# Kernel optimization log

Measured on AMD Instinct MI355X. Metric: run time of the kernel, lower is better.

Reference implementation:

```python
import jax, jax.numpy as jnp
import numpy as np

D_MODEL = 1024
NHEAD = 16
D_HEAD = D_MODEL // NHEAD
D_FF = 2 * D_MODEL
EPS = 1e-5


def setup_inputs() -> dict:
    key = jax.random.key(0)
    ks = jax.random.split(key, 12)
    s = 1.0 / np.sqrt(D_MODEL)
    x = jax.random.normal(ks[0], (4, 1024, D_MODEL), dtype=jnp.float32)
    # per-head projections stacked: [H, d_model, d_head] (x @ W layout)
    wq = jax.random.normal(ks[1], (NHEAD, D_MODEL, D_HEAD), dtype=jnp.float32) * s
    bq = jnp.zeros((NHEAD, D_HEAD), dtype=jnp.float32)
    wk = jax.random.normal(ks[2], (NHEAD, D_MODEL, D_HEAD), dtype=jnp.float32) * s
    bk = jnp.zeros((NHEAD, D_HEAD), dtype=jnp.float32)
    wv = jax.random.normal(ks[3], (NHEAD, D_MODEL, D_HEAD), dtype=jnp.float32) * s
    bv = jnp.zeros((NHEAD, D_HEAD), dtype=jnp.float32)
    wo_w = jax.random.normal(ks[4], (D_MODEL, D_MODEL), dtype=jnp.float32) * s
    wo_b = jnp.zeros((D_MODEL,), dtype=jnp.float32)
    ff1_w = jax.random.normal(ks[5], (D_MODEL, D_FF), dtype=jnp.float32) * s
    ff1_b = jnp.zeros((D_FF,), dtype=jnp.float32)
    ff2_w = jax.random.normal(ks[6], (D_FF, D_MODEL), dtype=jnp.float32) * (1.0 / np.sqrt(D_FF))
    ff2_b = jnp.zeros((D_MODEL,), dtype=jnp.float32)
    g1 = jnp.ones((D_MODEL,), dtype=jnp.float32)
    b1 = jnp.zeros((D_MODEL,), dtype=jnp.float32)
    g2 = jnp.ones((D_MODEL,), dtype=jnp.float32)
    b2 = jnp.zeros((D_MODEL,), dtype=jnp.float32)
    return dict(x=x, wq=wq, bq=bq, wk=wk, bk=bk, wv=wv, bv=bv,
                wo_w=wo_w, wo_b=wo_b, g1=g1, b1=b1,
                ff1_w=ff1_w, ff1_b=ff1_b, ff2_w=ff2_w, ff2_b=ff2_b,
                g2=g2, b2=b2)


def manual_layernorm(x, gamma, beta):
    # faithful to source: (x - mean) / (std + eps), std unbiased=False
    mean = jnp.mean(x, axis=-1, keepdims=True)
    std = jnp.sqrt(jnp.mean((x - mean) ** 2, axis=-1, keepdims=True))
    return gamma * (x - mean) / (std + EPS) + beta


def reference(x, wq, bq, wk, bk, wv, bv, wo_w, wo_b, g1, b1,
              ff1_w, ff1_b, ff2_w, ff2_b, g2, b2):
    B, S, D = x.shape
    # per-head projections, vectorized over heads: [B,H,S,d_head]
    q = jnp.einsum('bsd,hdk->bhsk', x, wq) + bq[None, :, None, :]
    k = jnp.einsum('bsd,hdk->bhsk', x, wk) + bk[None, :, None, :]
    v = jnp.einsum('bsd,hdk->bhsk', x, wv) + bv[None, :, None, :]
    scores = jnp.einsum('bhsk,bhtk->bhst', q, k) / jnp.sqrt(jnp.float32(D_HEAD))
    weights = jax.nn.softmax(scores, axis=-1)
    attn = jnp.einsum('bhst,bhtk->bhsk', weights, v)
    # concat heads back to [B,S,D]
    concat = jnp.transpose(attn, (0, 2, 1, 3)).reshape(B, S, D)
    proj = concat @ wo_w + wo_b
    h = manual_layernorm(x + proj, g1, b1)
    ff = jax.nn.relu(h @ ff1_w + ff1_b) @ ff2_w + ff2_b
    return manual_layernorm(h + ff, g2, b2)
```

## Files before the change

kernel.cpp:

```cpp
#include <hip/hip_runtime.h>
#include <hip/hip_bf16.h>

typedef __attribute__((ext_vector_type(8))) short bf16x8;
typedef __attribute__((ext_vector_type(4))) float f32x4;
using bf16 = __hip_bfloat16;

#define NTOK 4096
#define EPS_LN 1e-5f
#define QSCL 0.1803368801111244f

enum { EPI_F32 = 0, EPI_QKV = 1, EPI_RELU_BF16 = 2, EPI_BF16 = 3 };

#define VM8 asm volatile("s_waitcnt vmcnt(8)" ::: "memory")
#define VM0 asm volatile("s_waitcnt vmcnt(0)" ::: "memory")
#define LGKM0 asm volatile("s_waitcnt lgkmcnt(0)" ::: "memory")
#define SCHED0 __builtin_amdgcn_sched_barrier(0)
#define NOVM
#define DSRO(dst, ad, off) \
  asm volatile("ds_read_b128 %0, %1 offset:" #off : "=v"(dst) : "v"(ad))

__device__ inline void gload_lds16(const void* g, void* l) {
  __builtin_amdgcn_global_load_lds(
      (const __attribute__((address_space(1))) char*)g,
      (__attribute__((address_space(3))) char*)l, 16, 0, 0);
}

__device__ inline unsigned ldsoff(const void* p) {
  return (unsigned)(size_t)(const __attribute__((address_space(3))) char*)p;
}

__device__ inline unsigned short f2bfu(float x) {
  bf16 h = __float2bfloat16(x);
  return __builtin_bit_cast(unsigned short, h);
}
__device__ inline bf16 to_bf16(float v) { return __float2bfloat16(v); }
__device__ inline bf16 to_bf16(bf16 v) { return v; }

__device__ inline unsigned cvtpk(float lo, float hi) {
  unsigned r;
  asm volatile("v_cvt_pk_bf16_f32 %0, %1, %2" : "=v"(r) : "v"(lo), "v"(hi));
  return r;
}
__device__ inline float bu2f(unsigned short u) {
  unsigned v = (unsigned)u << 16;
  return __builtin_bit_cast(float, v);
}


__global__ __launch_bounds__(256) void cvt_bf16_kernel(const float* __restrict__ src,
                                                       bf16* __restrict__ dst, int n4) {
  int i = blockIdx.x * 256 + threadIdx.x;
  if (i >= n4) return;
  float4 v = ((const float4*)src)[i];
  ushort4 o;
  o.x = f2bfu(v.x); o.y = f2bfu(v.y); o.z = f2bfu(v.z); o.w = f2bfu(v.w);
  ((ushort4*)dst)[i] = o;
}

template <typename ST>
__global__ __launch_bounds__(256) void transpose_cvt(const ST* __restrict__ src,
                                                     bf16* __restrict__ dst, int R, int C) {
  __shared__ bf16 tile[32][33];
  int o = blockIdx.z;
  int r0 = blockIdx.y * 32, c0 = blockIdx.x * 32;
  int tx = threadIdx.x & 31, ty = threadIdx.x >> 5;
  const ST* s = src + (size_t)o * R * C;
  bf16* d = dst + (size_t)o * R * C;
#pragma unroll
  for (int i = 0; i < 32; i += 8)
    tile[ty + i][tx] = to_bf16(s[(size_t)(r0 + ty + i) * C + (c0 + tx)]);
  __syncthreads();
#pragma unroll
  for (int i = 0; i < 32; i += 8)
    d[(size_t)(c0 + ty + i) * R + (r0 + tx)] = tile[tx][ty + i];
}

__global__ __launch_bounds__(256) void pack_bias_kernel(const float* __restrict__ bq,
                                                        const float* __restrict__ bk,
                                                        const float* __restrict__ bv,
                                                        float* __restrict__ out) {
  int i = blockIdx.x * 256 + threadIdx.x;
  if (i >= 3072) return;
  out[i] = (i < 1024) ? bq[i] : (i < 2048 ? bk[i - 1024] : bv[i - 2048]);
}


#define STG(KOFF, DD) { _Pragma("unroll") for (int q = 0; q < 4; ++q) { \
    gload_lds16(gA0 + (KOFF) + (size_t)(q * 32) * lda2, \
                sAb + (DD) * 16384 + q * 4096 + w * 1024); \
    gload_lds16(gB0 + (KOFF) + (size_t)(q * 32) * ldb2, \
                sBb + (DD) * 16384 + q * 4096 + w * 1024); } }

#define TILE(OFFLIT, STG_, VMS) { \
  _Pragma("unroll") for (int i = 0; i < 4; ++i) { \
    DSRO(a[i][0], adA[i][0], OFFLIT); \
    DSRO(a[i][1], adA[i][1], OFFLIT); \
  } \
  _Pragma("unroll") for (int j = 0; j < 4; ++j) { \
    DSRO(b[j][0], adB[j][0], OFFLIT); \
    DSRO(b[j][1], adB[j][1], OFFLIT); \
  } \
  LGKM0; SCHED0; \
  __builtin_amdgcn_s_barrier(); \
  STG_; \
  __builtin_amdgcn_s_setprio(1); \
  _Pragma("unroll") for (int i = 0; i < 4; ++i) \
  _Pragma("unroll") for (int j = 0; j < 4; ++j) \
  _Pragma("unroll") for (int kk = 0; kk < 2; ++kk) \
    acc[i][j] = __builtin_amdgcn_mfma_f32_16x16x32_bf16( \
        a[i][kk], b[j][kk], acc[i][j], 0, 0, 0); \
  __builtin_amdgcn_s_setprio(0); \
  VMS; \
  __builtin_amdgcn_s_barrier(); }

__global__ __launch_bounds__(256, 2) void gemm128(
    const bf16* __restrict__ A, int lda,
    const bf16* __restrict__ Bt, int ldb,
    int M, int N, int K,
    int nbm, int nbn,
    const float* __restrict__ bias,
    float* __restrict__ Cf, bf16* __restrict__ Cb,
    bf16* __restrict__ Qd, bf16* __restrict__ Kd, bf16* __restrict__ Vd,
    int mode) {
  __shared__ bf16 sA[2][128][64];
  __shared__ bf16 sB[2][128][64];
  const int nwg = nbm * nbn;
  const int orig = blockIdx.x;
  const int wgid = (orig % 8) * (nwg / 8) + orig / 8;
  const int bm = wgid / nbn, bn = wgid % nbn;
  const int tid = threadIdx.x;
  const int w = tid >> 6, lane = tid & 63;
  const int wm = w >> 1, wn = w & 1;
  const int ri = lane & 15, kg = lane >> 4;
  const bf16* Ab = A + (size_t)bm * 128 * lda;
  const bf16* Bb = Bt + (size_t)bn * 128 * ldb;
  const int NT = K / 64;
  const size_t lda2 = (size_t)lda * 2, ldb2 = (size_t)ldb * 2;
  char* sAb = (char*)&sA[0][0][0];
  char* sBb = (char*)&sB[0][0][0];

  unsigned adA[4][2], adB[4][2];
  const unsigned sA0 = ldsoff(sAb), sB0 = ldsoff(sBb);
#pragma unroll
  for (int i = 0; i < 4; ++i) {
    int row = wm * 64 + i * 16 + ri;
    unsigned swz = (unsigned)((row & 7) << 4);
    adA[i][0] = sA0 + row * 128 + ((kg * 16) ^ swz);
    adA[i][1] = sA0 + row * 128 + ((64 + kg * 16) ^ swz);
  }
#pragma unroll
  for (int j = 0; j < 4; ++j) {
    int row = wn * 64 + j * 16 + ri;
    unsigned swz = (unsigned)((row & 7) << 4);
    adB[j][0] = sB0 + row * 128 + ((kg * 16) ^ swz);
    adB[j][1] = sB0 + row * 128 + ((64 + kg * 16) ^ swz);
  }

  const int r0 = tid >> 3;
  const int cb0 = ((tid & 7) * 16) ^ ((r0 & 7) << 4);
  const char* gA0 = (const char*)Ab + (size_t)r0 * lda2 + cb0;
  const char* gB0 = (const char*)Bb + (size_t)r0 * ldb2 + cb0;

  f32x4 acc[4][4] = {};
  bf16x8 a[4][2], b[4][2];

  STG(0, 0) STG(128, 1)
  VM8;
  __builtin_amdgcn_s_barrier();

  const int niter = NT / 2 - 1;
  for (int it = 0; it < niter; ++it) {
    TILE(0,     STG(256, 0), VM8)
    TILE(16384, STG(384, 1), VM8)
    gA0 += 256; gB0 += 256;
  }
  TILE(0,     , VM0)
  TILE(16384, , NOVM)

  const int colbase = bn * 128 + wn * 64 + ri;
  float bv4[4];
#pragma unroll
  for (int nf = 0; nf < 4; ++nf)
    bv4[nf] = bias ? bias[colbase + nf * 16] : 0.f;

  if (mode == EPI_QKV) {
    int col0 = bn * 128 + wn * 64;
    int which = col0 >> 10, hh = (col0 >> 6) & 15;
    bf16* dst = (which == 0) ? Qd : (which == 1) ? Kd : Vd;
    float scl = (which == 0) ? QSCL : 1.0f;
#pragma unroll
    for (int mf = 0; mf < 4; ++mf)
#pragma unroll
      for (int r = 0; r < 4; ++r) {
        int row = bm * 128 + wm * 64 + mf * 16 + kg * 4 + r;
        int b2 = row >> 10, s = row & 1023;
        bf16* o = dst + (((size_t)(b2 * 16 + hh)) * 1024 + s) * 64;
#pragma unroll
        for (int nf = 0; nf < 4; ++nf)
          o[nf * 16 + ri] = __float2bfloat16((acc[mf][nf][r] + bv4[nf]) * scl);
      }
  } else if (mode == EPI_F32) {
#pragma unroll
    for (int mf = 0; mf < 4; ++mf)
#pragma unroll
      for (int r = 0; r < 4; ++r) {
        int row = bm * 128 + wm * 64 + mf * 16 + kg * 4 + r;
        float* o = Cf + (size_t)row * N + colbase;
#pragma unroll
        for (int nf = 0; nf < 4; ++nf) o[nf * 16] = acc[mf][nf][r] + bv4[nf];
      }
  } else if (mode == EPI_RELU_BF16) {
#pragma unroll
    for (int mf = 0; mf < 4; ++mf)
#pragma unroll
      for (int r = 0; r < 4; ++r) {
        int row = bm * 128 + wm * 64 + mf * 16 + kg * 4 + r;
        bf16* o = Cb + (size_t)row * N + colbase;
#pragma unroll
        for (int nf = 0; nf < 4; ++nf) {
          float v = acc[mf][nf][r] + bv4[nf];
          o[nf * 16] = __float2bfloat16(v > 0.f ? v : 0.f);
        }
      }
  } else {
#pragma unroll
    for (int mf = 0; mf < 4; ++mf)
#pragma unroll
      for (int r = 0; r < 4; ++r) {
        int row = bm * 128 + wm * 64 + mf * 16 + kg * 4 + r;
        bf16* o = Cb + (size_t)row * N + colbase;
#pragma unroll
        for (int nf = 0; nf < 4; ++nf)
          o[nf * 16] = __float2bfloat16(acc[mf][nf][r] + bv4[nf]);
      }
  }
}

__global__ __launch_bounds__(256, 4) void attn_kernel(
    const bf16* __restrict__ Qb, const bf16* __restrict__ Kb,
    const bf16* __restrict__ Vs, bf16* __restrict__ Ob) {
  __shared__ bf16 KV[2][2][64][64];
  __shared__ bf16 Ps[4][16][64];
  const int orig = blockIdx.x;
  const int blk = (orig & 7) * 128 + (orig >> 3);
  const int bh = blk >> 4, qt = blk & 15;
  const int bb = bh >> 4, hh = bh & 15;
  const int tid = threadIdx.x, w = tid >> 6, lane = tid & 63;
  const int ri = lane & 15, kg = lane >> 4, r8 = lane >> 3;
  const int cb = ((lane & 7) * 16) ^ ((r8 & 7) << 4);
  const unsigned rsw = (unsigned)((ri & 7) << 4);
  const bf16* qp = Qb + (size_t)bh * 65536;
  const bf16* kp = Kb + (size_t)bh * 65536;
  const bf16* vp = Vs + (size_t)bh * 65536;
  const int q0 = qt * 64 + w * 16;
  const int c0 = w * 2, c1 = c0 + 1;

  unsigned offk0 = (unsigned)((kg * 16) ^ (int)rsw);
  unsigned offk1 = (unsigned)((64 + kg * 16) ^ (int)rsw);
  unsigned adF[4][2];
  const unsigned kv0 = ldsoff(&KV[0][0][0][0]);
#pragma unroll
  for (int n = 0; n < 4; ++n) {
    unsigned row = (unsigned)((n * 16 + ri) * 128);
    adF[n][0] = kv0 + row + offk0;
    adF[n][1] = kv0 + row + offk1;
  }
  const unsigned ps0 = ldsoff(&Ps[0][0][0]) + (unsigned)(w * 2048 + ri * 128);
  unsigned adPr[2] = {ps0 + offk0, ps0 + offk1};
  char* pwb = (char*)&Ps[0][0][0] + w * 2048 + ri * 128;
  char* adPw[4];
#pragma unroll
  for (int n = 0; n < 4; ++n)
    adPw[n] = pwb + ((n * 32 + kg * 8) ^ (int)rsw);

  bf16x8 qf[2];
  qf[0] = *(const bf16x8*)(qp + (size_t)(q0 + ri) * 64 + kg * 8);
  qf[1] = *(const bf16x8*)(qp + (size_t)(q0 + ri) * 64 + 32 + kg * 8);

  bf16x8 ones;
#pragma unroll
  for (int e = 0; e < 8; ++e) ones[e] = (short)0x3F80;

  f32x4 oacc[4] = {};
  f32x4 lacc = {};
  float mrun = -1e30f;

#define ASTAGE(T, D) { \
    gload_lds16((const char*)(kp + (size_t)((T) * 64 + c0 * 8 + r8) * 64) + cb, \
                (char*)KV + (D) * 16384 + c0 * 1024); \
    gload_lds16((const char*)(kp + (size_t)((T) * 64 + c1 * 8 + r8) * 64) + cb, \
                (char*)KV + (D) * 16384 + c1 * 1024); \
    gload_lds16((const char*)(vp + (size_t)(c0 * 8 + r8) * 1024 + (T) * 64) + cb, \
                (char*)KV + (D) * 16384 + 8192 + c0 * 1024); \
    gload_lds16((const char*)(vp + (size_t)(c1 * 8 + r8) * 1024 + (T) * 64) + cb, \
                (char*)KV + (D) * 16384 + 8192 + c1 * 1024); }

#define ATILE(KOFF, VOFF, STG_, ENDSYNC) { \
  bf16x8 kf0[4], kf1[4]; \
  _Pragma("unroll") for (int n = 0; n < 4; ++n) { \
    DSRO(kf0[n], adF[n][0], KOFF); \
    DSRO(kf1[n], adF[n][1], KOFF); \
  } \
  STG_; \
  LGKM0; SCHED0; \
  f32x4 sac[4] = {}; \
  _Pragma("unroll") for (int n = 0; n < 4; ++n) { \
    sac[n] = __builtin_amdgcn_mfma_f32_16x16x32_bf16(kf0[n], qf[0], sac[n], 0, 0, 0); \
    sac[n] = __builtin_amdgcn_mfma_f32_16x16x32_bf16(kf1[n], qf[1], sac[n], 0, 0, 0); \
  } \
  float mx[4]; \
  _Pragma("unroll") for (int n = 0; n < 4; ++n) \
    mx[n] = fmaxf(fmaxf(sac[n][0], sac[n][1]), fmaxf(sac[n][2], sac[n][3])); \
  float mt16 = fmaxf(fmaxf(mx[0], mx[1]), fmaxf(mx[2], mx[3])); \
  if (!__all(mt16 - mrun <= 8.f)) { \
    float mrow = fmaxf(mt16, __shfl_xor(mt16, 16)); \
    mrow = fmaxf(mrow, __shfl_xor(mrow, 32)); \
    float mnew = fmaxf(mrun, mrow); \
    float corr = exp2f(mrun - mnew); \
    mrun = mnew; \
    float cr[4]; \
    _Pragma("unroll") for (int r = 0; r < 4; ++r) cr[r] = __shfl(corr, kg * 4 + r); \
    _Pragma("unroll") for (int n = 0; n < 4; ++n) { \
      oacc[n][0] *= cr[0]; oacc[n][1] *= cr[1]; \
      oacc[n][2] *= cr[2]; oacc[n][3] *= cr[3]; \
    } \
    lacc[0] *= cr[0]; lacc[1] *= cr[1]; lacc[2] *= cr[2]; lacc[3] *= cr[3]; \
  } \
  _Pragma("unroll") for (int n = 0; n < 4; ++n) { \
    uint2 pk; \
    pk.x = cvtpk(exp2f(sac[n][0] - mrun), exp2f(sac[n][1] - mrun)); \
    pk.y = cvtpk(exp2f(sac[n][2] - mrun), exp2f(sac[n][3] - mrun)); \
    *(uint2*)adPw[n] = pk; \
  } \
  LGKM0; \
  bf16x8 pf0, pf1, vf0[4], vf1[4]; \
  DSRO(pf0, adPr[0], 0); \
  DSRO(pf1, adPr[1], 0); \
  _Pragma("unroll") for (int n = 0; n < 4; ++n) { \
    DSRO(vf0[n], adF[n][0], VOFF); \
    DSRO(vf1[n], adF[n][1], VOFF); \
  } \
  LGKM0; SCHED0; \
  _Pragma("unroll") for (int n = 0; n < 4; ++n) { \
    oacc[n] = __builtin_amdgcn_mfma_f32_16x16x32_bf16(pf0, vf0[n], oacc[n], 0, 0, 0); \
    oacc[n] = __builtin_amdgcn_mfma_f32_16x16x32_bf16(pf1, vf1[n], oacc[n], 0, 0, 0); \
  } \
  lacc = __builtin_amdgcn_mfma_f32_16x16x32_bf16(pf0, ones, lacc, 0, 0, 0); \
  lacc = __builtin_amdgcn_mfma_f32_16x16x32_bf16(pf1, ones, lacc, 0, 0, 0); \
  ENDSYNC }

#define SYNCT { VM0; __syncthreads(); }

  ASTAGE(0, 0);
  VM0;
  __syncthreads();

  for (int tt = 0; tt < 7; ++tt) {
    const int t2 = tt * 2;
    ATILE(0,     8192,  ASTAGE(t2 + 1, 1), SYNCT)
    ATILE(16384, 24576, ASTAGE(t2 + 2, 0), SYNCT)
  }
  ATILE(0,     8192,  ASTAGE(15, 1), SYNCT)
  ATILE(16384, 24576, ,              )

  float ivr[4];
#pragma unroll
  for (int r = 0; r < 4; ++r) ivr[r] = 1.f / lacc[r];
#pragma unroll
  for (int r = 0; r < 4; ++r) {
    int s = q0 + kg * 4 + r;
    size_t base = ((size_t)(bb * 1024 + s)) * 1024 + hh * 64;
#pragma unroll
    for (int n = 0; n < 4; ++n)
      Ob[base + n * 16 + ri] = __float2bfloat16(oacc[n][r] * ivr[r]);
  }
#undef ASTAGE
#undef ATILE
#undef SYNCT
}

__global__ __launch_bounds__(256) void ln_bb(
    const bf16* __restrict__ a, const bf16* __restrict__ b,
    const float* __restrict__ gamma, const float* __restrict__ beta,
    float* __restrict__ out_f32, bf16* __restrict__ out_bf16) {
  int row = blockIdx.x;
  int tid = threadIdx.x;
  ushort4 au = ((const ushort4*)(a + (size_t)row * 1024))[tid];
  ushort4 bu = ((const ushort4*)(b + (size_t)row * 1024))[tid];
  float4 z;
  z.x = bu2f(au.x) + bu2f(bu.x);
  z.y = bu2f(au.y) + bu2f(bu.y);
  z.z = bu2f(au.z) + bu2f(bu.z);
  z.w = bu2f(au.w) + bu2f(bu.w);
  float s = z.x + z.y + z.z + z.w;
  float ss = z.x * z.x + z.y * z.y + z.z * z.z + z.w * z.w;
#pragma unroll
  for (int o = 32; o >= 1; o >>= 1) { s += __shfl_xor(s, o); ss += __shfl_xor(ss, o); }
  __shared__ float red[8];
  int wid = tid >> 6;
  if ((tid & 63) == 0) { red[wid] = s; red[4 + wid] = ss; }
  __syncthreads();
  s = red[0] + red[1] + red[2] + red[3];
  ss = red[4] + red[5] + red[6] + red[7];
  float mean = s * (1.f / 1024.f);
  float var = ss * (1.f / 1024.f) - mean * mean;
  var = var > 0.f ? var : 0.f;
  float inv = 1.f / (sqrtf(var) + EPS_LN);
  float4 g = ((const float4*)gamma)[tid];
  float4 be = ((const float4*)beta)[tid];
  float4 y;
  y.x = (z.x - mean) * inv * g.x + be.x;
  y.y = (z.y - mean) * inv * g.y + be.y;
  y.z = (z.z - mean) * inv * g.z + be.z;
  y.w = (z.w - mean) * inv * g.w + be.w;
  ((float4*)(out_f32 + (size_t)row * 1024))[tid] = y;
  ushort4 o;
  o.x = f2bfu(y.x); o.y = f2bfu(y.y); o.z = f2bfu(y.z); o.w = f2bfu(y.w);
  ((ushort4*)(out_bf16 + (size_t)row * 1024))[tid] = o;
}

__global__ __launch_bounds__(256) void ln_fb(
    const float* __restrict__ a, const bf16* __restrict__ b,
    const float* __restrict__ gamma, const float* __restrict__ beta,
    float* __restrict__ out_f32) {
  int row = blockIdx.x;
  int tid = threadIdx.x;
  float4 av = ((const float4*)(a + (size_t)row * 1024))[tid];
  ushort4 bu = ((const ushort4*)(b + (size_t)row * 1024))[tid];
  float4 z;
  z.x = av.x + bu2f(bu.x);
  z.y = av.y + bu2f(bu.y);
  z.z = av.z + bu2f(bu.z);
  z.w = av.w + bu2f(bu.w);
  float s = z.x + z.y + z.z + z.w;
  float ss = z.x * z.x + z.y * z.y + z.z * z.z + z.w * z.w;
#pragma unroll
  for (int o = 32; o >= 1; o >>= 1) { s += __shfl_xor(s, o); ss += __shfl_xor(ss, o); }
  __shared__ float red[8];
  int wid = tid >> 6;
  if ((tid & 63) == 0) { red[wid] = s; red[4 + wid] = ss; }
  __syncthreads();
  s = red[0] + red[1] + red[2] + red[3];
  ss = red[4] + red[5] + red[6] + red[7];
  float mean = s * (1.f / 1024.f);
  float var = ss * (1.f / 1024.f) - mean * mean;
  var = var > 0.f ? var : 0.f;
  float inv = 1.f / (sqrtf(var) + EPS_LN);
  float4 g = ((const float4*)gamma)[tid];
  float4 be = ((const float4*)beta)[tid];
  float4 y;
  y.x = (z.x - mean) * inv * g.x + be.x;
  y.y = (z.y - mean) * inv * g.y + be.y;
  y.z = (z.z - mean) * inv * g.z + be.z;
  y.w = (z.w - mean) * inv * g.w + be.w;
  ((float4*)(out_f32 + (size_t)row * 1024))[tid] = y;
}

extern "C" void kernel_launch(void* const* d_in, const int* in_sizes, int n_in,
                              void* d_out, int out_size, void* d_ws, size_t ws_size,
                              hipStream_t stream) {
  const float* x = (const float*)d_in[0];
  const float* wq = (const float*)d_in[1];
  const float* bq = (const float*)d_in[2];
  const float* wk = (const float*)d_in[3];
  const float* bk = (const float*)d_in[4];
  const float* wv = (const float*)d_in[5];
  const float* bv = (const float*)d_in[6];
  const float* wo_w = (const float*)d_in[7];
  const float* wo_b = (const float*)d_in[8];
  const float* g1 = (const float*)d_in[9];
  const float* b1 = (const float*)d_in[10];
  const float* ff1w = (const float*)d_in[11];
  const float* ff1b = (const float*)d_in[12];
  const float* ff2w = (const float*)d_in[13];
  const float* ff2b = (const float*)d_in[14];
  const float* g2 = (const float*)d_in[15];
  const float* b2 = (const float*)d_in[16];

  char* ws = (char*)d_ws;
  size_t off = 0;
  auto alloc = [&](size_t bytes) {
    char* p = ws + off;
    off += (bytes + 255) & ~(size_t)255;
    return p;
  };
  bf16* xb = (bf16*)alloc((size_t)NTOK * 1024 * 2);
  bf16* wqkvt = (bf16*)alloc((size_t)3072 * 1024 * 2);
  bf16* wot = (bf16*)alloc((size_t)1024 * 1024 * 2);
  bf16* ff1t = (bf16*)alloc((size_t)2048 * 1024 * 2);
  bf16* ff2t = (bf16*)alloc((size_t)1024 * 2048 * 2);
  float* qkvbias = (float*)alloc(3072 * 4);
  bf16* qbuf = (bf16*)alloc((size_t)64 * 1024 * 64 * 2);
  bf16* kbuf = (bf16*)alloc((size_t)64 * 1024 * 64 * 2);
  bf16* vbuf = (bf16*)alloc((size_t)64 * 1024 * 64 * 2);
  bf16* vtb = (bf16*)alloc((size_t)64 * 64 * 1024 * 2);
  bf16* attnb = (bf16*)alloc((size_t)NTOK * 1024 * 2);
  bf16* projb = (bf16*)alloc((size_t)NTOK * 1024 * 2);
  bf16* hb = (bf16*)alloc((size_t)NTOK * 1024 * 2);
  bf16* ff1o = qbuf;
  float* hbuf = (float*)d_out;

  cvt_bf16_kernel<<<(NTOK * 1024 / 4 + 255) / 256, 256, 0, stream>>>(x, xb, NTOK * 1024 / 4);
  transpose_cvt<float><<<dim3(2, 32, 16), 256, 0, stream>>>(wq, wqkvt, 1024, 64);
  transpose_cvt<float><<<dim3(2, 32, 16), 256, 0, stream>>>(wk, wqkvt + 1024 * 1024, 1024, 64);
  transpose_cvt<float><<<dim3(2, 32, 16), 256, 0, stream>>>(wv, wqkvt + 2 * 1024 * 1024, 1024, 64);
  transpose_cvt<float><<<dim3(32, 32, 1), 256, 0, stream>>>(wo_w, wot, 1024, 1024);
  transpose_cvt<float><<<dim3(64, 32, 1), 256, 0, stream>>>(ff1w, ff1t, 1024, 2048);
  transpose_cvt<float><<<dim3(32, 64, 1), 256, 0, stream>>>(ff2w, ff2t, 2048, 1024);
  pack_bias_kernel<<<12, 256, 0, stream>>>(bq, bk, bv, qkvbias);

  gemm128<<<768, 256, 0, stream>>>(xb, 1024, wqkvt, 1024, 4096, 3072, 1024,
                                   32, 24, qkvbias,
                                   nullptr, nullptr, qbuf, kbuf, vbuf, EPI_QKV);
  transpose_cvt<bf16><<<dim3(2, 32, 64), 256, 0, stream>>>(vbuf, vtb, 1024, 64);
  attn_kernel<<<dim3(1024), 256, 0, stream>>>(qbuf, kbuf, vtb, attnb);
  gemm128<<<256, 256, 0, stream>>>(attnb, 1024, wot, 1024, 4096, 1024, 1024,
                                   32, 8, wo_b,
                                   nullptr, projb, nullptr, nullptr, nullptr, EPI_BF16);
  ln_bb<<<4096, 256, 0, stream>>>(xb, projb, g1, b1, hbuf, hb);
  gemm128<<<512, 256, 0, stream>>>(hb, 1024, ff1t, 1024, 4096, 2048, 1024,
                                   32, 16, ff1b,
                                   nullptr, ff1o, nullptr, nullptr, nullptr, EPI_RELU_BF16);
  gemm128<<<256, 256, 0, stream>>>(ff1o, 2048, ff2t, 2048, 4096, 1024, 2048,
                                   32, 8, ff2b,
                                   nullptr, projb, nullptr, nullptr, nullptr, EPI_BF16);
  ln_fb<<<4096, 256, 0, stream>>>(hbuf, projb, g2, b2, (float*)d_out);
}
```

Baseline: 167.3 us.

## Replace pipelined GEMM with single-buffer loop, add 128x64 GEMM, unify LayerNorm

The double-buffered, hand-scheduled GEMM main loop is replaced by a simple single-buffer loop that syncs every k-tile, with occupancy raised to 3 blocks. A new 128x64-tile GEMM is added for the N=1024 output projection and FF2 so they launch 512 blocks instead of 256. The second LayerNorm now reuses ln_bb and takes the bf16 h as its residual instead of the fp32 copy, and the fp32 h buffer is no longer written. Loads and MFMA no longer overlap, which risks exposing memory latency, and the residual path loses fp32 precision.

```diff
diff --git a/kernel.cpp b/kernel.cpp
--- a/kernel.cpp
+++ b/kernel.cpp
@@ -9,13 +9,11 @@
 #define EPS_LN 1e-5f
 #define QSCL 0.1803368801111244f
 
-enum { EPI_F32 = 0, EPI_QKV = 1, EPI_RELU_BF16 = 2, EPI_BF16 = 3 };
-
-#define VM8 asm volatile("s_waitcnt vmcnt(8)" ::: "memory")
-#define VM0 asm volatile("s_waitcnt vmcnt(0)" ::: "memory")
+enum { EPI_QKV = 1, EPI_RELU_BF16 = 2 };
+
 #define LGKM0 asm volatile("s_waitcnt lgkmcnt(0)" ::: "memory")
 #define SCHED0 __builtin_amdgcn_sched_barrier(0)
-#define NOVM
+#define VM0 asm volatile("s_waitcnt vmcnt(0)" ::: "memory")
 #define DSRO(dst, ad, off) \
   asm volatile("ds_read_b128 %0, %1 offset:" #off : "=v"(dst) : "v"(ad))
 
@@ -85,45 +83,20 @@
 }
 
 
-#define STG(KOFF, DD) { _Pragma("unroll") for (int q = 0; q < 4; ++q) { \
-    gload_lds16(gA0 + (KOFF) + (size_t)(q * 32) * lda2, \
-                sAb + (DD) * 16384 + q * 4096 + w * 1024); \
-    gload_lds16(gB0 + (KOFF) + (size_t)(q * 32) * ldb2, \
-                sBb + (DD) * 16384 + q * 4096 + w * 1024); } }
-
-#define TILE(OFFLIT, STG_, VMS) { \
-  _Pragma("unroll") for (int i = 0; i < 4; ++i) { \
-    DSRO(a[i][0], adA[i][0], OFFLIT); \
-    DSRO(a[i][1], adA[i][1], OFFLIT); \
-  } \
-  _Pragma("unroll") for (int j = 0; j < 4; ++j) { \
-    DSRO(b[j][0], adB[j][0], OFFLIT); \
-    DSRO(b[j][1], adB[j][1], OFFLIT); \
-  } \
-  LGKM0; SCHED0; \
-  __builtin_amdgcn_s_barrier(); \
-  STG_; \
-  __builtin_amdgcn_s_setprio(1); \
-  _Pragma("unroll") for (int i = 0; i < 4; ++i) \
-  _Pragma("unroll") for (int j = 0; j < 4; ++j) \
-  _Pragma("unroll") for (int kk = 0; kk < 2; ++kk) \
-    acc[i][j] = __builtin_amdgcn_mfma_f32_16x16x32_bf16( \
-        a[i][kk], b[j][kk], acc[i][j], 0, 0, 0); \
-  __builtin_amdgcn_s_setprio(0); \
-  VMS; \
-  __builtin_amdgcn_s_barrier(); }
-
-__global__ __launch_bounds__(256, 2) void gemm128(
+#define STG128(P) { _Pragma("unroll") for (int q = 0; q < 4; ++q) { \
+    gload_lds16(gA0 + (P) + (size_t)(q * 32) * lda2, sAb + q * 4096 + w * 1024); \
+    gload_lds16(gB0 + (P) + (size_t)(q * 32) * ldb2, sBb + q * 4096 + w * 1024); } }
+
+__global__ __launch_bounds__(256, 3) void gemm128(
     const bf16* __restrict__ A, int lda,
     const bf16* __restrict__ Bt, int ldb,
-    int M, int N, int K,
-    int nbm, int nbn,
+    int N, int K, int nbm, int nbn,
     const float* __restrict__ bias,
-    float* __restrict__ Cf, bf16* __restrict__ Cb,
+    bf16* __restrict__ Cb,
     bf16* __restrict__ Qd, bf16* __restrict__ Kd, bf16* __restrict__ Vd,
     int mode) {
-  __shared__ bf16 sA[2][128][64];
-  __shared__ bf16 sB[2][128][64];
+  __shared__ bf16 sA[128][64];
+  __shared__ bf16 sB[128][64];
   const int nwg = nbm * nbn;
   const int orig = blockIdx.x;
   const int wgid = (orig % 8) * (nwg / 8) + orig / 8;
@@ -132,56 +105,66 @@
   const int w = tid >> 6, lane = tid & 63;
   const int wm = w >> 1, wn = w & 1;
   const int ri = lane & 15, kg = lane >> 4;
-  const bf16* Ab = A + (size_t)bm * 128 * lda;
-  const bf16* Bb = Bt + (size_t)bn * 128 * ldb;
   const int NT = K / 64;
   const size_t lda2 = (size_t)lda * 2, ldb2 = (size_t)ldb * 2;
-  char* sAb = (char*)&sA[0][0][0];
-  char* sBb = (char*)&sB[0][0][0];
-
-  unsigned adA[4][2], adB[4][2];
-  const unsigned sA0 = ldsoff(sAb), sB0 = ldsoff(sBb);
+  char* sAb = (char*)&sA[0][0];
+  char* sBb = (char*)&sB[0][0];
+
+  const char* pA[4][2];
+  const char* pB[4][2];
 #pragma unroll
   for (int i = 0; i < 4; ++i) {
     int row = wm * 64 + i * 16 + ri;
-    unsigned swz = (unsigned)((row & 7) << 4);
-    adA[i][0] = sA0 + row * 128 + ((kg * 16) ^ swz);
-    adA[i][1] = sA0 + row * 128 + ((64 + kg * 16) ^ swz);
+    int swz = (row & 7) << 4;
+    pA[i][0] = sAb + row * 128 + ((kg * 16) ^ swz);
+    pA[i][1] = sAb + row * 128 + ((64 + kg * 16) ^ swz);
   }
 #pragma unroll
   for (int j = 0; j < 4; ++j) {
     int row = wn * 64 + j * 16 + ri;
-    unsigned swz = (unsigned)((row & 7) << 4);
-    adB[j][0] = sB0 + row * 128 + ((kg * 16) ^ swz);
-    adB[j][1] = sB0 + row * 128 + ((64 + kg * 16) ^ swz);
+    int swz = (row & 7) << 4;
+    pB[j][0] = sBb + row * 128 + ((kg * 16) ^ swz);
+    pB[j][1] = sBb + row * 128 + ((64 + kg * 16) ^ swz);
   }
 
   const int r0 = tid >> 3;
   const int cb0 = ((tid & 7) * 16) ^ ((r0 & 7) << 4);
-  const char* gA0 = (const char*)Ab + (size_t)r0 * lda2 + cb0;
-  const char* gB0 = (const char*)Bb + (size_t)r0 * ldb2 + cb0;
+  const char* gA0 = (const char*)(A + (size_t)bm * 128 * lda) + (size_t)r0 * lda2 + cb0;
+  const char* gB0 = (const char*)(Bt + (size_t)bn * 128 * ldb) + (size_t)r0 * ldb2 + cb0;
 
   f32x4 acc[4][4] = {};
-  bf16x8 a[4][2], b[4][2];
-
-  STG(0, 0) STG(128, 1)
-  VM8;
-  __builtin_amdgcn_s_barrier();
-
-  const int niter = NT / 2 - 1;
-  for (int it = 0; it < niter; ++it) {
-    TILE(0,     STG(256, 0), VM8)
-    TILE(16384, STG(384, 1), VM8)
-    gA0 += 256; gB0 += 256;
-  }
-  TILE(0,     , VM0)
-  TILE(16384, , NOVM)
+
+  size_t koff = 0;
+  for (int t = 0; t < NT; ++t) {
+    STG128(koff);
+    koff += 128;
+    __syncthreads();
+    bf16x8 a[4][2], b[4][2];
+#pragma unroll
+    for (int i = 0; i < 4; ++i) {
+      a[i][0] = *(const bf16x8*)pA[i][0];
+      a[i][1] = *(const bf16x8*)pA[i][1];
+    }
+#pragma unroll
+    for (int j = 0; j < 4; ++j) {
+      b[j][0] = *(const bf16x8*)pB[j][0];
+      b[j][1] = *(const bf16x8*)pB[j][1];
+    }
+#pragma unroll
+    for (int i = 0; i < 4; ++i)
+#pragma unroll
+      for (int j = 0; j < 4; ++j)
+#pragma unroll
+        for (int kk = 0; kk < 2; ++kk)
+          acc[i][j] = __builtin_amdgcn_mfma_f32_16x16x32_bf16(
+              a[i][kk], b[j][kk], acc[i][j], 0, 0, 0);
+    __syncthreads();
+  }
 
   const int colbase = bn * 128 + wn * 64 + ri;
   float bv4[4];
 #pragma unroll
-  for (int nf = 0; nf < 4; ++nf)
-    bv4[nf] = bias ? bias[colbase + nf * 16] : 0.f;
+  for (int nf = 0; nf < 4; ++nf) bv4[nf] = bias[colbase + nf * 16];
 
   if (mode == EPI_QKV) {
     int col0 = bn * 128 + wn * 64;
@@ -199,17 +182,7 @@
         for (int nf = 0; nf < 4; ++nf)
           o[nf * 16 + ri] = __float2bfloat16((acc[mf][nf][r] + bv4[nf]) * scl);
       }
-  } else if (mode == EPI_F32) {
-#pragma unroll
-    for (int mf = 0; mf < 4; ++mf)
-#pragma unroll
-      for (int r = 0; r < 4; ++r) {
-        int row = bm * 128 + wm * 64 + mf * 16 + kg * 4 + r;
-        float* o = Cf + (size_t)row * N + colbase;
-#pragma unroll
-        for (int nf = 0; nf < 4; ++nf) o[nf * 16] = acc[mf][nf][r] + bv4[nf];
-      }
-  } else if (mode == EPI_RELU_BF16) {
+  } else {
 #pragma unroll
     for (int mf = 0; mf < 4; ++mf)
 #pragma unroll
@@ -222,18 +195,101 @@
           o[nf * 16] = __float2bfloat16(v > 0.f ? v : 0.f);
         }
       }
-  } else {
-#pragma unroll
-    for (int mf = 0; mf < 4; ++mf)
-#pragma unroll
-      for (int r = 0; r < 4; ++r) {
-        int row = bm * 128 + wm * 64 + mf * 16 + kg * 4 + r;
-        bf16* o = Cb + (size_t)row * N + colbase;
-#pragma unroll
-        for (int nf = 0; nf < 4; ++nf)
-          o[nf * 16] = __float2bfloat16(acc[mf][nf][r] + bv4[nf]);
-      }
-  }
+  }
+}
+
+#define STG64(P) { \
+  _Pragma("unroll") for (int q = 0; q < 4; ++q) \
+    gload_lds16(gA0 + (P) + (size_t)(q * 32) * lda2, sAb + q * 4096 + w * 1024); \
+  _Pragma("unroll") for (int q = 0; q < 2; ++q) \
+    gload_lds16(gB0 + (P) + (size_t)(q * 32) * ldb2, sBb + q * 4096 + w * 1024); }
+
+__global__ __launch_bounds__(256, 3) void gemm64(
+    const bf16* __restrict__ A, int lda,
+    const bf16* __restrict__ Bt, int ldb,
+    int N, int K, int nbm, int nbn,
+    const float* __restrict__ bias,
+    bf16* __restrict__ Cb) {
+  __shared__ bf16 sA[128][64];
+  __shared__ bf16 sB[64][64];
+  const int nwg = nbm * nbn;
+  const int orig = blockIdx.x;
+  const int wgid = (orig % 8) * (nwg / 8) + orig / 8;
+  const int bm = wgid / nbn, bn = wgid % nbn;
+  const int tid = threadIdx.x;
+  const int w = tid >> 6, lane = tid & 63;
+  const int wm = w >> 1, wn = w & 1;
+  const int ri = lane & 15, kg = lane >> 4;
+  const int NT = K / 64;
+  const size_t lda2 = (size_t)lda * 2, ldb2 = (size_t)ldb * 2;
+  char* sAb = (char*)&sA[0][0];
+  char* sBb = (char*)&sB[0][0];
+
+  const char* pA[4][2];
+  const char* pB[2][2];
+#pragma unroll
+  for (int i = 0; i < 4; ++i) {
+    int row = wm * 64 + i * 16 + ri;
+    int swz = (row & 7) << 4;
+    pA[i][0] = sAb + row * 128 + ((kg * 16) ^ swz);
+    pA[i][1] = sAb + row * 128 + ((64 + kg * 16) ^ swz);
+  }
+#pragma unroll
+  for (int j = 0; j < 2; ++j) {
+    int row = wn * 32 + j * 16 + ri;
+    int swz = (row & 7) << 4;
+    pB[j][0] = sBb + row * 128 + ((kg * 16) ^ swz);
+    pB[j][1] = sBb + row * 128 + ((64 + kg * 16) ^ swz);
+  }
+
+  const int r0 = tid >> 3;
+  const int cb0 = ((tid & 7) * 16) ^ ((r0 & 7) << 4);
+  const char* gA0 = (const char*)(A + (size_t)bm * 128 * lda) + (size_t)r0 * lda2 + cb0;
+  const char* gB0 = (const char*)(Bt + (size_t)bn * 64 * ldb) + (size_t)r0 * ldb2 + cb0;
+
+  f32x4 acc[4][2] = {};
+
+  size_t koff = 0;
+  for (int t = 0; t < NT; ++t) {
+    STG64(koff);
+    koff += 128;
+    __syncthreads();
+    bf16x8 a[4][2], b[2][2];
+#pragma unroll
+    for (int i = 0; i < 4; ++i) {
+      a[i][0] = *(const bf16x8*)pA[i][0];
+      a[i][1] = *(const bf16x8*)pA[i][1];
+    }
+#pragma unroll
+    for (int j = 0; j < 2; ++j) {
+      b[j][0] = *(const bf16x8*)pB[j][0];
+      b[j][1] = *(const bf16x8*)pB[j][1];
+    }
+#pragma unroll
+    for (int i = 0; i < 4; ++i)
+#pragma unroll
+      for (int j = 0; j < 2; ++j)
+#pragma unroll
+        for (int kk = 0; kk < 2; ++kk)
+          acc[i][j] = __builtin_amdgcn_mfma_f32_16x16x32_bf16(
+              a[i][kk], b[j][kk], acc[i][j], 0, 0, 0);
+    __syncthreads();
+  }
+
+  const int colbase = bn * 64 + wn * 32 + ri;
+  float bv2[2];
+#pragma unroll
+  for (int nf = 0; nf < 2; ++nf) bv2[nf] = bias[colbase + nf * 16];
+#pragma unroll
+  for (int mf = 0; mf < 4; ++mf)
+#pragma unroll
+    for (int r = 0; r < 4; ++r) {
+      int row = bm * 128 + wm * 64 + mf * 16 + kg * 4 + r;
+      bf16* o = Cb + (size_t)row * N + colbase;
+#pragma unroll
+      for (int nf = 0; nf < 2; ++nf)
+        o[nf * 16] = __float2bfloat16(acc[mf][nf][r] + bv2[nf]);
+    }
 }
 
 __global__ __launch_bounds__(256, 4) void attn_kernel(
@@ -413,47 +469,13 @@
   y.y = (z.y - mean) * inv * g.y + be.y;
   y.z = (z.z - mean) * inv * g.z + be.z;
   y.w = (z.w - mean) * inv * g.w + be.w;
-  ((float4*)(out_f32 + (size_t)row * 1024))[tid] = y;
-  ushort4 o;
-  o.x = f2bfu(y.x); o.y = f2bfu(y.y); o.z = f2bfu(y.z); o.w = f2bfu(y.w);
-  ((ushort4*)(out_bf16 + (size_t)row * 1024))[tid] = o;
-}
-
-__global__ __launch_bounds__(256) void ln_fb(
-    const float* __restrict__ a, const bf16* __restrict__ b,
-    const float* __restrict__ gamma, const float* __restrict__ beta,
-    float* __restrict__ out_f32) {
-  int row = blockIdx.x;
-  int tid = threadIdx.x;
-  float4 av = ((const float4*)(a + (size_t)row * 1024))[tid];
-  ushort4 bu = ((const ushort4*)(b + (size_t)row * 1024))[tid];
-  float4 z;
-  z.x = av.x + bu2f(bu.x);
-  z.y = av.y + bu2f(bu.y);
-  z.z = av.z + bu2f(bu.z);
-  z.w = av.w + bu2f(bu.w);
-  float s = z.x + z.y + z.z + z.w;
-  float ss = z.x * z.x + z.y * z.y + z.z * z.z + z.w * z.w;
-#pragma unroll
-  for (int o = 32; o >= 1; o >>= 1) { s += __shfl_xor(s, o); ss += __shfl_xor(ss, o); }
-  __shared__ float red[8];
-  int wid = tid >> 6;
-  if ((tid & 63) == 0) { red[wid] = s; red[4 + wid] = ss; }
-  __syncthreads();
-  s = red[0] + red[1] + red[2] + red[3];
-  ss = red[4] + red[5] + red[6] + red[7];
-  float mean = s * (1.f / 1024.f);
-  float var = ss * (1.f / 1024.f) - mean * mean;
-  var = var > 0.f ? var : 0.f;
-  float inv = 1.f / (sqrtf(var) + EPS_LN);
-  float4 g = ((const float4*)gamma)[tid];
-  float4 be = ((const float4*)beta)[tid];
-  float4 y;
-  y.x = (z.x - mean) * inv * g.x + be.x;
-  y.y = (z.y - mean) * inv * g.y + be.y;
-  y.z = (z.z - mean) * inv * g.z + be.z;
-  y.w = (z.w - mean) * inv * g.w + be.w;
-  ((float4*)(out_f32 + (size_t)row * 1024))[tid] = y;
+  if (out_f32)
+    ((float4*)(out_f32 + (size_t)row * 1024))[tid] = y;
+  if (out_bf16) {
+    ushort4 o;
+    o.x = f2bfu(y.x); o.y = f2bfu(y.y); o.z = f2bfu(y.z); o.w = f2bfu(y.w);
+    ((ushort4*)(out_bf16 + (size_t)row * 1024))[tid] = o;
+  }
 }
 
 extern "C" void kernel_launch(void* const* d_in, const int* in_sizes, int n_in,
@@ -498,7 +520,6 @@
   bf16* projb = (bf16*)alloc((size_t)NTOK * 1024 * 2);
   bf16* hb = (bf16*)alloc((size_t)NTOK * 1024 * 2);
   bf16* ff1o = qbuf;
-  float* hbuf = (float*)d_out;
 
   cvt_bf16_kernel<<<(NTOK * 1024 / 4 + 255) / 256, 256, 0, stream>>>(x, xb, NTOK * 1024 / 4);
   transpose_cvt<float><<<dim3(2, 32, 16), 256, 0, stream>>>(wq, wqkvt, 1024, 64);
@@ -509,20 +530,16 @@
   transpose_cvt<float><<<dim3(32, 64, 1), 256, 0, stream>>>(ff2w, ff2t, 2048, 1024);
   pack_bias_kernel<<<12, 256, 0, stream>>>(bq, bk, bv, qkvbias);
 
-  gemm128<<<768, 256, 0, stream>>>(xb, 1024, wqkvt, 1024, 4096, 3072, 1024,
-                                   32, 24, qkvbias,
-                                   nullptr, nullptr, qbuf, kbuf, vbuf, EPI_QKV);
+  gemm128<<<768, 256, 0, stream>>>(xb, 1024, wqkvt, 1024, 3072, 1024, 32, 24,
+                                   qkvbias, nullptr, qbuf, kbuf, vbuf, EPI_QKV);
   transpose_cvt<bf16><<<dim3(2, 32, 64), 256, 0, stream>>>(vbuf, vtb, 1024, 64);
   attn_kernel<<<dim3(1024), 256, 0, stream>>>(qbuf, kbuf, vtb, attnb);
-  gemm128<<<256, 256, 0, stream>>>(attnb, 1024, wot, 1024, 4096, 1024, 1024,
-                                   32, 8, wo_b,
-                                   nullptr, projb, nullptr, nullptr, nullptr, EPI_BF16);
-  ln_bb<<<4096, 256, 0, stream>>>(xb, projb, g1, b1, hbuf, hb);
-  gemm128<<<512, 256, 0, stream>>>(hb, 1024, ff1t, 1024, 4096, 2048, 1024,
-                                   32, 16, ff1b,
-                                   nullptr, ff1o, nullptr, nullptr, nullptr, EPI_RELU_BF16);
-  gemm128<<<256, 256, 0, stream>>>(ff1o, 2048, ff2t, 2048, 4096, 1024, 2048,
-                                   32, 8, ff2b,
-                                   nullptr, projb, nullptr, nullptr, nullptr, EPI_BF16);
-  ln_fb<<<4096, 256, 0, stream>>>(hbuf, projb, g2, b2, (float*)d_out);
-}
+  gemm64<<<512, 256, 0, stream>>>(attnb, 1024, wot, 1024, 1024, 1024, 32, 16,
+                                  wo_b, projb);
+  ln_bb<<<4096, 256, 0, stream>>>(xb, projb, g1, b1, nullptr, hb);
+  gemm128<<<512, 256, 0, stream>>>(hb, 1024, ff1t, 1024, 2048, 1024, 32, 16,
+                                   ff1b, ff1o, nullptr, nullptr, nullptr, EPI_RELU_BF16);
+  gemm64<<<512, 256, 0, stream>>>(ff1o, 2048, ff2t, 2048, 1024, 2048, 32, 16,
+                                  ff2b, projb);
+  ln_bb<<<4096, 256, 0, stream>>>(hb, projb, g2, b2, (float*)d_out, nullptr);
+}
```

New measurement: 177.0 us (median of 2 runs). +5.8%, slower.
